# Performance work log

Measured on AMD Instinct MI355X. Metric: run time of the kernel, lower is better.

The kernel has to match this reference:

```python
import jax, jax.numpy as jnp
import numpy as np

N = 50000      # n_nodes
E = 800000     # edges (before self-loops)
IN = 128       # in_dim
HID = 32       # hidden_dim (per-head out channels)
HEADS = 4
EMB = 128      # embed_dim
LAYERS = 3
NEG_SLOPE = 0.2  # PyG GATv2 default leaky_relu slope


def _layer_norm(x, g, b):
    mu = jnp.mean(x, axis=-1, keepdims=True)
    var = jnp.var(x, axis=-1, keepdims=True)
    return g * (x - mu) / jnp.sqrt(var + 1e-5) + b


def _gatv2(h, src, dst, n, Wl, bl, Wr, br, att, bias):
    # GATv2Conv (PyG semantics, share_weights=False, concat=True).
    H, C = att.shape
    xl = (h @ Wl + bl).reshape(n, H, C)   # target (i) transform
    xr = (h @ Wr + br).reshape(n, H, C)   # source (j) transform
    x_i = xl[dst]                          # [Etot, H, C] gather
    x_j = xr[src]
    e = jax.nn.leaky_relu(x_i + x_j, NEG_SLOPE)
    logit = jnp.einsum('ehc,hc->eh', e, att)          # [Etot, H]
    # segment softmax over destination node (every node has a self-loop)
    m = jax.ops.segment_max(logit, dst, num_segments=n)
    ex = jnp.exp(logit - m[dst])
    den = jax.ops.segment_sum(ex, dst, num_segments=n)
    alpha = ex / (den[dst] + 1e-16)
    out = jax.ops.segment_sum(alpha[..., None] * x_j, dst, num_segments=n)
    return out.reshape(n, H * C) + bias


def setup_inputs() -> dict:
    key = jax.random.key(0)
    ks = iter(jax.random.split(key, 64))
    d = {}
    d['x'] = jax.random.normal(next(ks), (N, IN), jnp.float32)
    d['edge_index'] = jax.random.randint(next(ks), (2, E), 0, N, dtype=jnp.int64)

    def w(shape, fan):
        return jax.random.normal(next(ks), shape, jnp.float32) / np.float32(np.sqrt(fan))

    HC = HID * HEADS
    d['W_in'] = w((IN, HID), IN); d['b_in'] = jnp.zeros((HID,), jnp.float32)
    for i in range(LAYERS):
        ic = HID if i == 0 else HC
        d[f'Wl{i}'] = w((ic, HC), ic); d[f'bl{i}'] = jnp.zeros((HC,), jnp.float32)
        d[f'Wr{i}'] = w((ic, HC), ic); d[f'br{i}'] = jnp.zeros((HC,), jnp.float32)
        d[f'att{i}'] = w((HEADS, HID), HID)
        d[f'bo{i}'] = jnp.zeros((HC,), jnp.float32)
        d[f'g{i}'] = jnp.ones((HC,), jnp.float32)
        d[f'be{i}'] = jnp.zeros((HC,), jnp.float32)
    d['W_out'] = w((HC, EMB), HC); d['b_out'] = jnp.zeros((EMB,), jnp.float32)
    return d


def reference(x, edge_index, W_in, b_in,
              Wl0, bl0, Wr0, br0, att0, bo0, g0, be0,
              Wl1, bl1, Wr1, br1, att1, bo1, g1, be1,
              Wl2, bl2, Wr2, br2, att2, bo2, g2, be2,
              W_out, b_out):
    n = x.shape[0]
    loops = jnp.arange(n, dtype=edge_index.dtype)  # add_self_loops=True
    src = jnp.concatenate([edge_index[0], loops])
    dst = jnp.concatenate([edge_index[1], loops])

    h = jax.nn.gelu(x @ W_in + b_in, approximate=False)
    layers = [(Wl0, bl0, Wr0, br0, att0, bo0, g0, be0),
              (Wl1, bl1, Wr1, br1, att1, bo1, g1, be1),
              (Wl2, bl2, Wr2, br2, att2, bo2, g2, be2)]
    for (Wl, bl, Wr, br, att, bo, g, be) in layers:
        h_new = jax.nn.gelu(_layer_norm(_gatv2(h, src, dst, n, Wl, bl, Wr, br, att, bo), g, be), approximate=False)
        h = h + h_new if h.shape == h_new.shape else h_new  # dropout = identity (eval)
    out = h @ W_out + b_out
    norm = jnp.maximum(jnp.linalg.norm(out, axis=-1, keepdims=True), 1e-12)
    return out / norm
```

## Files before the change

kernel.cpp:

```cpp
#include <hip/hip_runtime.h>
#include <hip/hip_bf16.h>
#include <math.h>

#define N_NODES 50000
#define N_EDGES 800000
#define IN_DIM  128
#define HC_DIM  128
#define HID_C   32
#define SCAN_NB 196
#define LOG2E   1.4426950408889634f

typedef __attribute__((ext_vector_type(8))) short short8;
typedef __attribute__((ext_vector_type(4))) float f32x4;
typedef _Float16 hf8 __attribute__((ext_vector_type(8)));
typedef unsigned int uint4v __attribute__((ext_vector_type(4)));

__device__ __forceinline__ float gelu_f(float x){
    return 0.5f*x*(1.0f + erff(x*0.7071067811865475f));
}

__device__ __forceinline__ void split2(float f, short& h, short& l){
    __hip_bfloat16 bh = __float2bfloat16(f);
    float r = f - __bfloat162float(bh);
    __hip_bfloat16 blo = __float2bfloat16(r);
    h = *reinterpret_cast<short*>(&bh);
    l = *reinterpret_cast<short*>(&blo);
}
__device__ __forceinline__ unsigned short f2h(float f){
    _Float16 h = (_Float16)f;
    return __builtin_bit_cast(unsigned short, h);
}
__device__ __forceinline__ float bf2f(unsigned short u){
    return __uint_as_float(((unsigned)u)<<16);
}

__global__ __launch_bounds__(256) void k_count(const int* __restrict__ dst, int* __restrict__ cnt,
                                               int* __restrict__ rank){
    int b = blockIdx.x*1024 + threadIdx.x;
    #pragma unroll
    for(int i=0;i<4;i++){
        int e = b + i*256;
        if(e < N_EDGES) rank[e] = atomicAdd(&cnt[dst[e]], 1);
    }
}

__global__ __launch_bounds__(256) void k_scan1(const int* __restrict__ cnt, int* __restrict__ rowptr,
                                               int* __restrict__ part){
    __shared__ int sh[256];
    int t=threadIdx.x; int i=blockIdx.x*256+t;
    int v = (i<N_NODES)? cnt[i] : 0;
    sh[t]=v; __syncthreads();
    for(int off=1; off<256; off<<=1){
        int y = (t>=off)? sh[t-off] : 0;
        __syncthreads();
        sh[t] += y;
        __syncthreads();
    }
    if(i<N_NODES) rowptr[i] = sh[t]-v;
    if(t==255) part[blockIdx.x] = sh[255];
}

__global__ __launch_bounds__(256) void k_scan2(int* __restrict__ part){
    __shared__ int sh[256];
    int t=threadIdx.x;
    int v = (t<SCAN_NB)? part[t] : 0;
    sh[t]=v; __syncthreads();
    for(int off=1; off<256; off<<=1){
        int y=(t>=off)? sh[t-off]:0;
        __syncthreads();
        sh[t]+=y;
        __syncthreads();
    }
    if(t<SCAN_NB) part[t] = sh[t]-v;
}

__global__ __launch_bounds__(256) void k_scan3(int* __restrict__ rowptr, const int* __restrict__ part){
    int t=threadIdx.x; int i=blockIdx.x*256+t;
    if(i<N_NODES) rowptr[i] += part[blockIdx.x];
    if(i==0) rowptr[N_NODES]=N_EDGES;
}

__global__ __launch_bounds__(256) void k_fill(const int* __restrict__ src, const int* __restrict__ dst,
                                              const int* __restrict__ rowptr, const int* __restrict__ rank,
                                              int* __restrict__ col){
    int b = blockIdx.x*1024 + threadIdx.x;
    #pragma unroll
    for(int i=0;i<4;i++){
        int e = b + i*256;
        if(e < N_EDGES) col[rowptr[dst[e]] + rank[e]] = src[e];
    }
}

__global__ __launch_bounds__(256) void k_splitW(const float* __restrict__ W0, const float* __restrict__ W1,
                                                const float* __restrict__ W2, const float* __restrict__ W3,
                                                const float* __restrict__ W4, const float* __restrict__ W5,
                                                const float* __restrict__ W6, short* __restrict__ WT){
    int bx = blockIdx.x;
    int m, kc;
    if(bx < 2){ m = bx; kc = 0; }
    else { m = 2 + (bx-2)/4; kc = (bx-2)&3; }
    const float* src; int K; size_t off;
    switch(m){
        case 0: src=W0; K=32;  off=0;      break;
        case 1: src=W1; K=32;  off=8192;   break;
        case 2: src=W2; K=128; off=16384;  break;
        case 3: src=W3; K=128; off=49152;  break;
        case 4: src=W4; K=128; off=81920;  break;
        case 5: src=W5; K=128; off=114688; break;
        default:src=W6; K=128; off=147456; break;
    }
    short* hi = WT + off;
    short* lo = hi + (size_t)K*HC_DIM;
    #pragma unroll
    for(int i=0;i<16;i++){
        int idx = threadIdx.x + i*256;
        int k = kc*32 + (idx>>7);
        int n = idx & 127;
        float f = src[(size_t)k*HC_DIM + n];
        short h,l; split2(f,h,l);
        hi[(size_t)n*K + k] = h;
        lo[(size_t)n*K + k] = l;
    }
}

__global__ __launch_bounds__(256) void k_gemm_in(const float* __restrict__ x, const float* __restrict__ W,
                                                 const float* __restrict__ b,
                                                 short* __restrict__ hhi, short* __restrict__ hlo){
    int id = blockIdx.x*256+threadIdx.x;
    int r = id>>5, c = id&31;
    const float4* x4 = (const float4*)(x + (size_t)r*IN_DIM);
    float acc=0.f;
    #pragma unroll 8
    for(int k=0;k<IN_DIM/4;k++){
        float4 xv = x4[k];
        acc = fmaf(xv.x, W[(4*k  )*HID_C+c], acc);
        acc = fmaf(xv.y, W[(4*k+1)*HID_C+c], acc);
        acc = fmaf(xv.z, W[(4*k+2)*HID_C+c], acc);
        acc = fmaf(xv.w, W[(4*k+3)*HID_C+c], acc);
    }
    float v = gelu_f(acc + b[c]);
    short hh,ll; split2(v,hh,ll);
    hhi[(size_t)r*HID_C+c] = hh;
    hlo[(size_t)r*HID_C+c] = ll;
}

template<int K, bool PAIR, bool NORM>
__global__ __launch_bounds__(256) void k_mm(const short* __restrict__ Ahi, const short* __restrict__ Alo,
                                            const short* __restrict__ WTl, const float* __restrict__ bl,
                                            const short* __restrict__ WTr, const float* __restrict__ br,
                                            float* __restrict__ XLf, unsigned short* __restrict__ XLh,
                                            unsigned short* __restrict__ XR16){
    constexpr int LDS_K = 40;
    constexpr int NCH = K / 32;
    __shared__ short As_hi[64*LDS_K], As_lo[64*LDS_K];
    __shared__ short Bh0[128*LDS_K], Bl0[128*LDS_K];
    __shared__ short Bh1[PAIR?128*LDS_K:1], Bl1[PAIR?128*LDS_K:1];
    __shared__ float ssq[NORM?256:1];

    int t = threadIdx.x;
    int lane = t & 63, wave = t >> 6;
    int quad = lane >> 4, ml = lane & 15;
    int rbase = blockIdx.x * 64;

    const short* WTl_lo = WTl + (size_t)K*HC_DIM;
    const short* WTr_lo = PAIR ? (WTr + (size_t)K*HC_DIM) : nullptr;

    f32x4 accL[4][2], accR[4][2];
    #pragma unroll
    for(int i=0;i<4;i++)
        #pragma unroll
        for(int j=0;j<2;j++){ accL[i][j]=(f32x4){0,0,0,0}; accR[i][j]=(f32x4){0,0,0,0}; }

    int r = t >> 2, seg = t & 3;
    int gr = rbase + r; if(gr >= N_NODES) gr = N_NODES-1;

    for(int c=0; c<NCH; c++){
        if(c) __syncthreads();
        size_t ka = (size_t)gr*K + c*32 + seg*8;
        *(short8*)(As_hi + r*LDS_K + seg*8) = *(const short8*)(Ahi + ka);
        *(short8*)(As_lo + r*LDS_K + seg*8) = *(const short8*)(Alo + ka);
        #pragma unroll
        for(int u=0; u<2; u++){
            int uu = t + u*256;
            int n = uu >> 2, sg = uu & 3;
            size_t kw = (size_t)n*K + c*32 + sg*8;
            *(short8*)(Bh0 + n*LDS_K + sg*8) = *(const short8*)(WTl + kw);
            *(short8*)(Bl0 + n*LDS_K + sg*8) = *(const short8*)(WTl_lo + kw);
            if(PAIR){
                *(short8*)(Bh1 + n*LDS_K + sg*8) = *(const short8*)(WTr + kw);
                *(short8*)(Bl1 + n*LDS_K + sg*8) = *(const short8*)(WTr_lo + kw);
            }
        }
        __syncthreads();

        int k0 = quad*8;
        short8 ah[4], al[4];
        #pragma unroll
        for(int i=0;i<4;i++){
            ah[i] = *(const short8*)(As_hi + (16*i + ml)*LDS_K + k0);
            al[i] = *(const short8*)(As_lo + (16*i + ml)*LDS_K + k0);
        }
        #pragma unroll
        for(int j=0;j<2;j++){
            int nrow = j*64 + wave*16 + ml;
            short8 bh = *(const short8*)(Bh0 + nrow*LDS_K + k0);
            short8 blo = *(const short8*)(Bl0 + nrow*LDS_K + k0);
            #pragma unroll
            for(int i=0;i<4;i++){
                accL[i][j] = __builtin_amdgcn_mfma_f32_16x16x32_bf16(ah[i], bh,  accL[i][j], 0,0,0);
                accL[i][j] = __builtin_amdgcn_mfma_f32_16x16x32_bf16(ah[i], blo, accL[i][j], 0,0,0);
                accL[i][j] = __builtin_amdgcn_mfma_f32_16x16x32_bf16(al[i], bh,  accL[i][j], 0,0,0);
            }
            if(PAIR){
                short8 ch = *(const short8*)(Bh1 + nrow*LDS_K + k0);
                short8 cl = *(const short8*)(Bl1 + nrow*LDS_K + k0);
                #pragma unroll
                for(int i=0;i<4;i++){
                    accR[i][j] = __builtin_amdgcn_mfma_f32_16x16x32_bf16(ah[i], ch, accR[i][j], 0,0,0);
                    accR[i][j] = __builtin_amdgcn_mfma_f32_16x16x32_bf16(ah[i], cl, accR[i][j], 0,0,0);
                    accR[i][j] = __builtin_amdgcn_mfma_f32_16x16x32_bf16(al[i], ch, accR[i][j], 0,0,0);
                }
            }
        }
    }

    int col0 = wave*16 + ml, col1 = 64 + wave*16 + ml;
    float bL0 = bl[col0], bL1 = bl[col1];

    if(NORM){
        #pragma unroll
        for(int i=0;i<4;i++){
            #pragma unroll
            for(int rr=0;rr<4;rr++){
                float v0 = accL[i][0][rr] + bL0;
                float v1 = accL[i][1][rr] + bL1;
                float p = v0*v0 + v1*v1;
                p += __shfl_xor(p,1); p += __shfl_xor(p,2);
                p += __shfl_xor(p,4); p += __shfl_xor(p,8);
                if(ml==0) ssq[wave*64 + 16*i + quad*4 + rr] = p;
            }
        }
        __syncthreads();
        #pragma unroll
        for(int i=0;i<4;i++){
            #pragma unroll
            for(int rr=0;rr<4;rr++){
                int row = 16*i + quad*4 + rr;
                int grr = rbase + row;
                if(grr < N_NODES){
                    float tot = ssq[row] + ssq[64+row] + ssq[128+row] + ssq[192+row];
                    float inv = 1.0f / fmaxf(sqrtf(tot), 1e-12f);
                    XLf[(size_t)grr*HC_DIM + col0] = (accL[i][0][rr] + bL0) * inv;
                    XLf[(size_t)grr*HC_DIM + col1] = (accL[i][1][rr] + bL1) * inv;
                }
            }
        }
    } else {
        float bR0 = PAIR ? br[col0] : 0.f, bR1 = PAIR ? br[col1] : 0.f;
        #pragma unroll
        for(int i=0;i<4;i++){
            #pragma unroll
            for(int rr=0;rr<4;rr++){
                int grr = rbase + 16*i + quad*4 + rr;
                if(grr < N_NODES){
                    XLh[(size_t)grr*HC_DIM + col0] = f2h(accL[i][0][rr] + bL0);
                    XLh[(size_t)grr*HC_DIM + col1] = f2h(accL[i][1][rr] + bL1);
                    if(PAIR){
                        XR16[(size_t)grr*HC_DIM + col0] = f2h(accR[i][0][rr] + bR0);
                        XR16[(size_t)grr*HC_DIM + col1] = f2h(accR[i][1][rr] + bR1);
                    }
                }
            }
        }
    }
}

__global__ __launch_bounds__(256) void k_node(const unsigned short* __restrict__ XLH, const unsigned short* __restrict__ XR,
    const int* __restrict__ rowptr, const int* __restrict__ colidx,
    const float* __restrict__ att, const float* __restrict__ bo,
    const float* __restrict__ gg, const float* __restrict__ be,
    const short* __restrict__ hold_hi, const short* __restrict__ hold_lo,
    short* __restrict__ hi_out, short* __restrict__ lo_out)
{
    int wave=threadIdx.x>>6, lane=threadIdx.x&63;
    int qd = lane >> 4, cl = lane & 15;
    int c8 = cl << 3;
    int ch2 = c8 + (qd<<1);

    float4 aa = *(const float4*)(att + c8);
    float4 abv = *(const float4*)(att + c8 + 4);
    float af[8] = {aa.x,aa.y,aa.z,aa.w,abv.x,abv.y,abv.z,abv.w};
    hf8 av6, av4;
    const float s6 = 0.6f*LOG2E, s4 = 0.4f*LOG2E;
    #pragma unroll
    for(int k=0;k<8;k++){
        av6[k] = (_Float16)(af[k]*s6);
        av4[k] = (_Float16)(af[k]*s4);
    }
    float4 b0 = *(const float4*)(bo + c8);
    float4 b1 = *(const float4*)(bo + c8 + 4);
    float bof[8] = {b0.x,b0.y,b0.z,b0.w,b1.x,b1.y,b1.z,b1.w};
    float2 g2  = *(const float2*)(gg + ch2);
    float2 be2 = *(const float2*)(be + ch2);

    #define H2(v,k) __builtin_shufflevector(v, v, 2*(k), 2*(k)+1)
    #define LOADH(j, xv) { xv = *(const hf8*)((const _Float16*)XR + ((size_t)((unsigned)(j)<<7)) + c8); }
#if defined(__has_builtin) && __has_builtin(__builtin_amdgcn_fdot2)
    #define LOGIT(xv, q) { \
        hf8 u_ = xlh + xv; \
        hf8 a_ = __builtin_bit_cast(hf8, __builtin_bit_cast(uint4v, u_) & 0x7fff7fffu); \
        float qa_ = __builtin_amdgcn_fdot2(H2(u_,0), H2(av6,0), 0.f, false); \
        float qb_ = __builtin_amdgcn_fdot2(H2(a_,0), H2(av4,0), 0.f, false); \
        qa_ = __builtin_amdgcn_fdot2(H2(u_,1), H2(av6,1), qa_, false); \
        qb_ = __builtin_amdgcn_fdot2(H2(a_,1), H2(av4,1), qb_, false); \
        qa_ = __builtin_amdgcn_fdot2(H2(u_,2), H2(av6,2), qa_, false); \
        qb_ = __builtin_amdgcn_fdot2(H2(a_,2), H2(av4,2), qb_, false); \
        qa_ = __builtin_amdgcn_fdot2(H2(u_,3), H2(av6,3), qa_, false); \
        qb_ = __builtin_amdgcn_fdot2(H2(a_,3), H2(av4,3), qb_, false); \
        q = qa_ + qb_; \
        q += __shfl_xor(q,1); q += __shfl_xor(q,2); }
#else
    #define LOGIT(xv, q) { \
        hf8 u_ = xlh + xv; \
        hf8 a_ = __builtin_bit_cast(hf8, __builtin_bit_cast(uint4v, u_) & 0x7fff7fffu); \
        q = 0.f; \
        _Pragma("unroll") \
        for(int k_=0;k_<8;k_++) q = fmaf((float)u_[k_], (float)av6[k_], fmaf((float)a_[k_], (float)av4[k_], q)); \
        q += __shfl_xor(q,1); q += __shfl_xor(q,2); }
#endif
    #define UPDATE4 { \
        float nm = fmaxf(m, fmaxf(fmaxf(q0,q1),fmaxf(q2,q3))); \
        float sc = exp2f(m-nm); \
        float e0=exp2f(q0-nm), e1=exp2f(q1-nm), e2=exp2f(q2-nm), e3=exp2f(q3-nm); \
        ls = fmaf(ls, sc, (e0+e1)+(e2+e3)); \
        _Pragma("unroll") \
        for(int k=0;k<8;k++) \
            acc[k] = fmaf(acc[k], sc, fmaf(e0,(float)x0[k], fmaf(e1,(float)x1[k], fmaf(e2,(float)x2[k], e3*(float)x3[k])))); \
        m = nm; }

    int nstep = gridDim.x << 2;
    for(int node = (blockIdx.x<<2) + wave; node < N_NODES; node += nstep){

        int beg = rowptr[node], end = rowptr[node+1];
        hf8 xlh = *(const hf8*)((const _Float16*)XLH + ((size_t)((unsigned)node<<7)) + c8);
        hf8 xs; LOADH(node, xs)
        float hres0 = 0.f, hres1 = 0.f;
        if(hold_hi){
            short2 hh = *(const short2*)(hold_hi + (size_t)node*HC_DIM + ch2);
            short2 hl = *(const short2*)(hold_lo + (size_t)node*HC_DIM + ch2);
            hres0 = bf2f((unsigned short)hh.x) + bf2f((unsigned short)hl.x);
            hres1 = bf2f((unsigned short)hh.y) + bf2f((unsigned short)hl.y);
        }

        float qs; LOGIT(xs, qs)
        float m, ls, acc[8];
        if(qd==0){
            m = qs; ls = 1.f;
            #pragma unroll
            for(int k=0;k<8;k++) acc[k] = (float)xs[k];
        } else {
            m = -1e30f; ls = 0.f;
            #pragma unroll
            for(int k=0;k<8;k++) acc[k] = 0.f;
        }

        int P = end - beg;
        int nb = P >> 4;
        int base = beg;
        int qoff = qd << 2;
        for(int b=0; b<nb; b++, base += 16){
            int b2 = base + qoff;
            int j0 = colidx[b2], j1 = colidx[b2+1], j2 = colidx[b2+2], j3 = colidx[b2+3];
            hf8 x0,x1,x2,x3;
            LOADH(j0,x0) LOADH(j1,x1) LOADH(j2,x2) LOADH(j3,x3)
            float q0,q1,q2,q3;
            LOGIT(x0,q0) LOGIT(x1,q1) LOGIT(x2,q2) LOGIT(x3,q3)
            UPDATE4
        }
        if(base < end){
            int b2 = base + qoff;
            int j0 = (b2  <end)? colidx[b2]   : node;
            int j1 = (b2+1<end)? colidx[b2+1] : node;
            int j2 = (b2+2<end)? colidx[b2+2] : node;
            int j3 = (b2+3<end)? colidx[b2+3] : node;
            hf8 x0,x1,x2,x3;
            LOADH(j0,x0) LOADH(j1,x1) LOADH(j2,x2) LOADH(j3,x3)
            float q0,q1,q2,q3;
            LOGIT(x0,q0) LOGIT(x1,q1) LOGIT(x2,q2) LOGIT(x3,q3)
            if(b2+1>=end) q1 = -INFINITY;
            if(b2+2>=end) q2 = -INFINITY;
            if(b2+3>=end) q3 = -INFINITY;
            if(b2 < end){
                UPDATE4
            }
        }

        #pragma unroll
        for(int mk=16; mk<=32; mk<<=1){
            float mo  = __shfl_xor(m, mk);
            float lso = __shfl_xor(ls, mk);
            float ao[8];
            #pragma unroll
            for(int k=0;k<8;k++) ao[k] = __shfl_xor(acc[k], mk);
            float nm = fmaxf(m, mo);
            float s0 = exp2f(m-nm), s1 = exp2f(mo-nm);
            ls = ls*s0 + lso*s1;
            #pragma unroll
            for(int k=0;k<8;k++) acc[k] = acc[k]*s0 + ao[k]*s1;
            m = nm;
        }

        float inv = 1.0f/ls;
        float o[8];
        #pragma unroll
        for(int k=0;k<8;k++) o[k] = fmaf(acc[k], inv, bof[k]);
        float s1v = ((o[0]+o[1])+(o[2]+o[3])) + ((o[4]+o[5])+(o[6]+o[7]));
        float s2v = o[0]*o[0];
        #pragma unroll
        for(int k=1;k<8;k++) s2v = fmaf(o[k],o[k],s2v);
        #pragma unroll
        for(int mk=1;mk<16;mk<<=1){ s1v += __shfl_xor(s1v,mk); s2v += __shfl_xor(s2v,mk); }
        float mean = s1v*(1.f/128.f);
        float var  = s2v*(1.f/128.f) - mean*mean;
        float rstd = rsqrtf(var + 1e-5f);

        float oa = (qd&2) ? ((qd&1)? o[6] : o[4]) : ((qd&1)? o[2] : o[0]);
        float ob = (qd&2) ? ((qd&1)? o[7] : o[5]) : ((qd&1)? o[3] : o[1]);
        float r0 = gelu_f(fmaf(g2.x*(oa-mean), rstd, be2.x)) + hres0;
        float r1 = gelu_f(fmaf(g2.y*(ob-mean), rstd, be2.y)) + hres1;
        short h0,l0,h1,l1;
        split2(r0,h0,l0); split2(r1,h1,l1);
        *(short2*)(hi_out + (size_t)node*HC_DIM + ch2) = make_short2(h0,h1);
        *(short2*)(lo_out + (size_t)node*HC_DIM + ch2) = make_short2(l0,l1);
    }
    #undef UPDATE4
    #undef LOGIT
    #undef LOADH
    #undef H2
}

extern "C" void kernel_launch(void* const* d_in, const int* in_sizes, int n_in,
                              void* d_out, int out_size, void* d_ws, size_t ws_size,
                              hipStream_t stream)
{
    const float* x   = (const float*)d_in[0];
    const int*   ei  = (const int*)  d_in[1];
    const float* Win = (const float*)d_in[2];
    const float* bin = (const float*)d_in[3];
    const float *Wl[3], *bl[3], *Wr[3], *br[3], *att[3], *bo[3], *gg[3], *be[3];
    for(int i=0;i<3;i++){
        const int base = 4 + 8*i;
        Wl[i]=(const float*)d_in[base+0]; bl[i]=(const float*)d_in[base+1];
        Wr[i]=(const float*)d_in[base+2]; br[i]=(const float*)d_in[base+3];
        att[i]=(const float*)d_in[base+4]; bo[i]=(const float*)d_in[base+5];
        gg[i]=(const float*)d_in[base+6]; be[i]=(const float*)d_in[base+7];
    }
    const float* Wout=(const float*)d_in[28];
    const float* bout=(const float*)d_in[29];
    float* out = (float*)d_out;

    char* w = (char*)d_ws;
    unsigned short* XLH = (unsigned short*)w; w += (size_t)N_NODES*HC_DIM*2;
    unsigned short* XR16 = (unsigned short*)w; w += (size_t)N_NODES*HC_DIM*2;
    short* hAhi = (short*)w; w += (size_t)N_NODES*HC_DIM*2;
    short* hAlo = (short*)w; w += (size_t)N_NODES*HC_DIM*2;
    short* hBhi = (short*)w; w += (size_t)N_NODES*HC_DIM*2;
    short* hBlo = (short*)w; w += (size_t)N_NODES*HC_DIM*2;
    short* WT   = (short*)w; w += (size_t)180224*2;
    int* rowptr = (int*)w;  w += (size_t)(N_NODES+2)*4;
    int* cursor = (int*)w;  w += (size_t)N_NODES*4;
    int* colidx = (int*)w;  w += (size_t)N_EDGES*4;
    int* rank   = (int*)w;  w += (size_t)N_EDGES*4;
    int* part   = (int*)w;  w += 256*4;

    const int* srcp = ei;
    const int* dstp = ei + N_EDGES;

    const short* WTl0 = WT + 0;      const short* WTr0 = WT + 8192;
    const short* WTl1 = WT + 16384;  const short* WTr1 = WT + 49152;
    const short* WTl2 = WT + 81920;  const short* WTr2 = WT + 114688;
    const short* WTo  = WT + 147456;

    k_splitW<<<22,256,0,stream>>>(Wl[0],Wr[0],Wl[1],Wr[1],Wl[2],Wr[2],Wout, WT);
    hipMemsetAsync(cursor, 0, (size_t)N_NODES*4, stream);
    k_count <<<782,256, 0, stream>>>(dstp, cursor, rank);
    k_scan1 <<<SCAN_NB,256,0,stream>>>(cursor, rowptr, part);
    k_scan2 <<<1,   256, 0, stream>>>(part);
    k_scan3 <<<SCAN_NB,256,0,stream>>>(rowptr, part);
    k_fill  <<<782,256, 0, stream>>>(srcp, dstp, rowptr, rank, colidx);
    k_gemm_in<<<6250,256,0,stream>>>(x, Win, bin, hAhi, hAlo);

    k_mm<32,true,false><<<782,256,0,stream>>>(hAhi, hAlo, WTl0, bl[0], WTr0, br[0],
                                              nullptr, XLH, XR16);
    k_node<<<2048,256,0,stream>>>(XLH,XR16,rowptr,colidx,att[0],bo[0],gg[0],be[0],
                                  (const short*)nullptr, (const short*)nullptr, hBhi, hBlo);

    k_mm<128,true,false><<<782,256,0,stream>>>(hBhi, hBlo, WTl1, bl[1], WTr1, br[1],
                                               nullptr, XLH, XR16);
    k_node<<<2048,256,0,stream>>>(XLH,XR16,rowptr,colidx,att[1],bo[1],gg[1],be[1],
                                  hBhi, hBlo, hAhi, hAlo);

    k_mm<128,true,false><<<782,256,0,stream>>>(hAhi, hAlo, WTl2, bl[2], WTr2, br[2],
                                               nullptr, XLH, XR16);
    k_node<<<2048,256,0,stream>>>(XLH,XR16,rowptr,colidx,att[2],bo[2],gg[2],be[2],
                                  hAhi, hAlo, hBhi, hBlo);

    k_mm<128,false,true><<<782,256,0,stream>>>(hBhi, hBlo, WTo, bout, nullptr, nullptr,
                                               out, nullptr, nullptr);
}
```

Measured before the change: 505.2 us.

## Read GEMM weight fragments straight from global and fix node kernel grid

The GEMM kernel no longer stages the weight hi/lo tiles in shared memory. Each wave now reads its B fragments directly from global memory, which cuts LDS usage and raises occupancy but issues more uncoalesced global loads that depend on cache hits. The node-aggregation kernel moves from a grid-stride loop over 2048 blocks to exactly 6250 blocks, with each wave handling two nodes 25000 apart. That reduces loop overhead and fixes the per-wave work at two nodes.

```diff
diff --git a/kernel.cpp b/kernel.cpp
--- a/kernel.cpp
+++ b/kernel.cpp
@@ -9,6 +9,7 @@
 #define HID_C   32
 #define SCAN_NB 196
 #define LOG2E   1.4426950408889634f
+#define NODE_HALF 25000
 
 typedef __attribute__((ext_vector_type(8))) short short8;
 typedef __attribute__((ext_vector_type(4))) float f32x4;
@@ -153,8 +154,6 @@
     constexpr int LDS_K = 40;
     constexpr int NCH = K / 32;
     __shared__ short As_hi[64*LDS_K], As_lo[64*LDS_K];
-    __shared__ short Bh0[128*LDS_K], Bl0[128*LDS_K];
-    __shared__ short Bh1[PAIR?128*LDS_K:1], Bl1[PAIR?128*LDS_K:1];
     __shared__ float ssq[NORM?256:1];
 
     int t = threadIdx.x;
@@ -179,21 +178,10 @@
         size_t ka = (size_t)gr*K + c*32 + seg*8;
         *(short8*)(As_hi + r*LDS_K + seg*8) = *(const short8*)(Ahi + ka);
         *(short8*)(As_lo + r*LDS_K + seg*8) = *(const short8*)(Alo + ka);
-        #pragma unroll
-        for(int u=0; u<2; u++){
-            int uu = t + u*256;
-            int n = uu >> 2, sg = uu & 3;
-            size_t kw = (size_t)n*K + c*32 + sg*8;
-            *(short8*)(Bh0 + n*LDS_K + sg*8) = *(const short8*)(WTl + kw);
-            *(short8*)(Bl0 + n*LDS_K + sg*8) = *(const short8*)(WTl_lo + kw);
-            if(PAIR){
-                *(short8*)(Bh1 + n*LDS_K + sg*8) = *(const short8*)(WTr + kw);
-                *(short8*)(Bl1 + n*LDS_K + sg*8) = *(const short8*)(WTr_lo + kw);
-            }
-        }
         __syncthreads();
 
         int k0 = quad*8;
+        size_t kg = (size_t)(c*32 + quad*8);
         short8 ah[4], al[4];
         #pragma unroll
         for(int i=0;i<4;i++){
@@ -203,8 +191,8 @@
         #pragma unroll
         for(int j=0;j<2;j++){
             int nrow = j*64 + wave*16 + ml;
-            short8 bh = *(const short8*)(Bh0 + nrow*LDS_K + k0);
-            short8 blo = *(const short8*)(Bl0 + nrow*LDS_K + k0);
+            short8 bh  = *(const short8*)(WTl    + (size_t)nrow*K + kg);
+            short8 blo = *(const short8*)(WTl_lo + (size_t)nrow*K + kg);
             #pragma unroll
             for(int i=0;i<4;i++){
                 accL[i][j] = __builtin_amdgcn_mfma_f32_16x16x32_bf16(ah[i], bh,  accL[i][j], 0,0,0);
@@ -212,8 +200,8 @@
                 accL[i][j] = __builtin_amdgcn_mfma_f32_16x16x32_bf16(al[i], bh,  accL[i][j], 0,0,0);
             }
             if(PAIR){
-                short8 ch = *(const short8*)(Bh1 + nrow*LDS_K + k0);
-                short8 cl = *(const short8*)(Bl1 + nrow*LDS_K + k0);
+                short8 ch = *(const short8*)(WTr    + (size_t)nrow*K + kg);
+                short8 cl = *(const short8*)(WTr_lo + (size_t)nrow*K + kg);
                 #pragma unroll
                 for(int i=0;i<4;i++){
                     accR[i][j] = __builtin_amdgcn_mfma_f32_16x16x32_bf16(ah[i], ch, accR[i][j], 0,0,0);
@@ -338,8 +326,10 @@
             acc[k] = fmaf(acc[k], sc, fmaf(e0,(float)x0[k], fmaf(e1,(float)x1[k], fmaf(e2,(float)x2[k], e3*(float)x3[k])))); \
         m = nm; }
 
-    int nstep = gridDim.x << 2;
-    for(int node = (blockIdx.x<<2) + wave; node < N_NODES; node += nstep){
+    int nbase = (blockIdx.x<<2) + wave;
+    #pragma unroll 1
+    for(int rep=0; rep<2; rep++){
+        int node = nbase + rep*NODE_HALF;
 
         int beg = rowptr[node], end = rowptr[node+1];
         hf8 xlh = *(const hf8*)((const _Float16*)XLH + ((size_t)((unsigned)node<<7)) + c8);
@@ -492,17 +482,17 @@
 
     k_mm<32,true,false><<<782,256,0,stream>>>(hAhi, hAlo, WTl0, bl[0], WTr0, br[0],
                                               nullptr, XLH, XR16);
-    k_node<<<2048,256,0,stream>>>(XLH,XR16,rowptr,colidx,att[0],bo[0],gg[0],be[0],
+    k_node<<<6250,256,0,stream>>>(XLH,XR16,rowptr,colidx,att[0],bo[0],gg[0],be[0],
                                   (const short*)nullptr, (const short*)nullptr, hBhi, hBlo);
 
     k_mm<128,true,false><<<782,256,0,stream>>>(hBhi, hBlo, WTl1, bl[1], WTr1, br[1],
                                                nullptr, XLH, XR16);
-    k_node<<<2048,256,0,stream>>>(XLH,XR16,rowptr,colidx,att[1],bo[1],gg[1],be[1],
+    k_node<<<6250,256,0,stream>>>(XLH,XR16,rowptr,colidx,att[1],bo[1],gg[1],be[1],
                                   hBhi, hBlo, hAhi, hAlo);
 
     k_mm<128,true,false><<<782,256,0,stream>>>(hAhi, hAlo, WTl2, bl[2], WTr2, br[2],
                                                nullptr, XLH, XR16);
-    k_node<<<2048,256,0,stream>>>(XLH,XR16,rowptr,colidx,att[2],bo[2],gg[2],be[2],
+    k_node<<<6250,256,0,stream>>>(XLH,XR16,rowptr,colidx,att[2],bo[2],gg[2],be[2],
                                   hAhi, hAlo, hBhi, hBlo);
 
     k_mm<128,false,true><<<782,256,0,stream>>>(hBhi, hBlo, WTo, bout, nullptr, nullptr,
```

Result: slower. 519.5 us (+2.8%).
